# Optimization experiments

Measured on AMD Instinct MI355X. Metric: run time of the kernel, lower is better.

## Reference

```python
import jax, jax.numpy as jnp
import numpy as np

WAY = 5  # N_way from init


def setup_inputs() -> dict:
    key = jax.random.key(0)
    k1, k2, k3, k4 = jax.random.split(key, 4)
    N, c, h, w = 80, 2048, 16, 16
    S = 512  # shuffle_num
    x = jax.random.normal(k1, (N, c, h, w), dtype=jnp.float32)
    s_ca = jax.random.uniform(k2, (N, c, 1, 1), dtype=jnp.float32)
    # random channel indices per sample (stand-in for random.sample)
    rand_index = jax.random.randint(k3, (N, S), 0, c)
    # partner offset per sample (stand-in for random j != i)
    partner = jax.random.randint(k4, (N,), 0, N - 1)
    return {"x": x, "s_ca": s_ca, "rand_index": rand_index,
            "partner": partner, "shuffle_num": S}


def reference(x, s_ca, rand_index, partner, shuffle_num):
    N, c, h, w = x.shape
    way = WAY
    scores = s_ca.reshape(N, c)
    # per-sample top-k channels by attention score
    _, topk_idx = jax.lax.top_k(scores, shuffle_num)          # [N, S]
    # partner sample j != i (offset trick guarantees inequality)
    j = (jnp.arange(N) + 1 + partner) % N                      # [N]
    bi = jnp.arange(N)[:, None]                                # [N, 1]
    x_topk = x[bi, topk_idx]                                   # [N, S, h, w]
    x_part = x[j[:, None], rand_index]                         # [N, S, h, w]
    blend = 0.7 * x_topk + 0.3 * x_part
    # scatter blended channels back (batched gather-blend-scatter)
    aug_x = x.at[bi, topk_idx].set(blend)                      # [N, c, h, w]
    # group into (way, shot, ...) and concat original + augmented episodes
    x_r = x.reshape(way, -1, c, h, w)
    aug_r = aug_x.reshape(way, -1, c, h, w)
    out = jnp.concatenate((x_r, aug_r), axis=1)                # [way, 2*shot, c, h, w]
    s = s_ca.reshape(way, -1, c, 1, 1)
    s = jnp.concatenate((s, s), axis=1)                        # repeat(1,2,1,1,1)
    out = out * s
    return out.reshape(-1, c, h, w)                            # [2N, c, h, w]
```

## Files before the change

### kernel.cpp

```cpp
#include <hip/hip_runtime.h>

#define N_SAMP 80
#define C_CH   2048
#define HW     256
#define S_TOP  512
#define HW4    64

__global__ __launch_bounds__(256) void fused_shuffle_kernel(
    const float4* __restrict__ x4, const float* __restrict__ s_ca,
    const int* __restrict__ rand_index, const int* __restrict__ partner,
    float4* __restrict__ out4) {
  const unsigned int lane = threadIdx.x & 63u;
  const unsigned int wid = threadIdx.x >> 6;
  const unsigned int blk = blockIdx.x;
  const unsigned int n = blk >> 7;
  const unsigned int ch0 = ((blk & 127u) << 4) | (wid << 2);
  const unsigned int g = n >> 4;
  const unsigned int b = n & 15u;

  const float* __restrict__ row = s_ca + (size_t)n * C_CH;
  const float4* __restrict__ row4 = (const float4*)row;

  const float4 sq = row4[ch0 >> 2];
  const float si[4] = {sq.x, sq.y, sq.z, sq.w};

  int jn = (int)n + 1 + partner[n];
  if (jn >= N_SAMP) jn -= N_SAMP;

  float4 v[4];
#pragma unroll
  for (int c = 0; c < 4; ++c)
    v[c] = x4[(((size_t)n * C_CH + ch0 + c) << 6) | lane];

  unsigned long long kc[4];
#pragma unroll
  for (int c = 0; c < 4; ++c) {
    unsigned int bi = __float_as_uint(si[c]);
    bi ^= (bi & 0x80000000u) ? 0xFFFFFFFFu : 0x80000000u;
    kc[c] = ((unsigned long long)bi << 11) |
            (unsigned long long)(C_CH - 1 - (ch0 + c));
  }

  int cnt[4] = {0, 0, 0, 0};
#pragma unroll
  for (int q = 0; q < 8; ++q) {
    const float4 sv = row4[q * 64 + lane];
    const unsigned int j0 = 4u * (q * 64u + lane);
    unsigned long long kj[4];
#pragma unroll
    for (int e = 0; e < 4; ++e) {
      unsigned int bj = __float_as_uint((&sv.x)[e]);
      bj ^= (bj & 0x80000000u) ? 0xFFFFFFFFu : 0x80000000u;
      kj[e] = ((unsigned long long)bj << 11) |
              (unsigned long long)(C_CH - 1 - (j0 + e));
    }
#pragma unroll
    for (int c = 0; c < 4; ++c) {
#pragma unroll
      for (int e = 0; e < 4; ++e)
        cnt[c] += __popcll(__ballot(kj[e] > kc[c]));
    }
  }

  const size_t base_plain =
      (((size_t)((g << 5) | b) * C_CH + ch0) << 6) | lane;
  const size_t aug_off = ((size_t)(16 * C_CH)) << 6;

#pragma unroll
  for (int c = 0; c < 4; ++c) {
    const float s = si[c];
    float4 pv = make_float4(v[c].x * s, v[c].y * s, v[c].z * s, v[c].w * s);
    float4 av = pv;
    if (cnt[c] < S_TOP) {
      const int pc = rand_index[(size_t)n * S_TOP + cnt[c]];
      const float4 u = x4[((((size_t)jn << 11) | (size_t)pc) << 6) | lane];
      av.x = (0.7f * v[c].x + 0.3f * u.x) * s;
      av.y = (0.7f * v[c].y + 0.3f * u.y) * s;
      av.z = (0.7f * v[c].z + 0.3f * u.z) * s;
      av.w = (0.7f * v[c].w + 0.3f * u.w) * s;
    }
    out4[base_plain + ((size_t)c << 6)] = pv;
    out4[base_plain + aug_off + ((size_t)c << 6)] = av;
  }
}

extern "C" void kernel_launch(void* const* d_in, const int* in_sizes, int n_in,
                              void* d_out, int out_size, void* d_ws,
                              size_t ws_size, hipStream_t stream) {
  const float* x = (const float*)d_in[0];
  const float* s_ca = (const float*)d_in[1];
  const int* rand_index = (const int*)d_in[2];
  const int* partner = (const int*)d_in[3];

  const int nblocks = (N_SAMP * C_CH) / 16;
  fused_shuffle_kernel<<<nblocks, 256, 0, stream>>>(
      (const float4*)x, s_ca, rand_index, partner, (float4*)d_out);
}
```

Before: 445.7 us.

## Precompute per-sample top-k ranks via histogram bucket sort in a separate kernel

Moves the per-channel rank computation out of the streaming kernel into a per-sample kernel that buckets scores by value, sorts within buckets in shared memory, and writes a channel-to-partner-channel map to workspace. The streaming kernel then reads one index per channel instead of doing 128 wave ballots per wave. This removes redundant O(C) rank work repeated by every wave, at the cost of an extra launch and a low-parallelism 80-block prologue. Bucketing assumes scores spread over [0,1) for balanced buckets, but it remains correct for any values.

```diff
diff --git a/kernel.cpp b/kernel.cpp
--- a/kernel.cpp
+++ b/kernel.cpp
@@ -6,9 +6,91 @@
 #define S_TOP  512
 #define HW4    64
 
-__global__ __launch_bounds__(256) void fused_shuffle_kernel(
+__global__ __launch_bounds__(256) void rank_hist_kernel(
+    const float* __restrict__ s_ca, const int* __restrict__ rand_index,
+    int* __restrict__ pcmap) {
+  __shared__ unsigned int keys[C_CH];
+  __shared__ unsigned short bkt[C_CH];
+  __shared__ int hist[C_CH];
+  __shared__ int cumgt[C_CH];
+  __shared__ unsigned long long sorted[C_CH];
+  __shared__ int chunk[256];
+
+  const int n = blockIdx.x;
+  const int t = threadIdx.x;
+  const float* __restrict__ row = s_ca + (size_t)n * C_CH;
+
+  for (int i = t; i < C_CH; i += 256) hist[i] = 0;
+  __syncthreads();
+
+  for (int i = t; i < C_CH; i += 256) {
+    const float s = row[i];
+    unsigned int mb = __float_as_uint(s);
+    mb ^= (mb & 0x80000000u) ? 0xFFFFFFFFu : 0x80000000u;
+    keys[i] = mb;
+    int b = (int)(s * 2048.0f);
+    b = (b < 0) ? 0 : ((b > 2047) ? 2047 : b);
+    bkt[i] = (unsigned short)b;
+    atomicAdd(&hist[b], 1);
+  }
+  __syncthreads();
+
+  {
+    int cs = 0;
+#pragma unroll
+    for (int k = 0; k < 8; ++k) cs += hist[t * 8 + k];
+    chunk[t] = cs;
+  }
+  __syncthreads();
+  for (int d = 1; d < 256; d <<= 1) {
+    const int add = (t >= d) ? chunk[t - d] : 0;
+    __syncthreads();
+    chunk[t] += add;
+    __syncthreads();
+  }
+  const int total = chunk[255];
+
+  {
+    int run = total - chunk[t];
+#pragma unroll
+    for (int k = 7; k >= 0; --k) {
+      cumgt[t * 8 + k] = run;
+      run += hist[t * 8 + k];
+    }
+  }
+  __syncthreads();
+
+  for (int i = t; i < C_CH; i += 256) hist[i] = 0;
+  __syncthreads();
+
+  for (int i = t; i < C_CH; i += 256) {
+    const int b = bkt[i];
+    const unsigned long long key =
+        ((unsigned long long)keys[i] << 11) |
+        (unsigned long long)(C_CH - 1 - i);
+    const int pos = cumgt[b] + atomicAdd(&hist[b], 1);
+    sorted[pos] = key;
+  }
+  __syncthreads();
+
+  int* __restrict__ pm = pcmap + (size_t)n * C_CH;
+  const int* __restrict__ ri = rand_index + (size_t)n * S_TOP;
+  for (int i = t; i < C_CH; i += 256) {
+    const int b = bkt[i];
+    const int lo = cumgt[b];
+    const int nb = ((b > 0) ? cumgt[b - 1] : total) - lo;
+    const unsigned long long mykey =
+        ((unsigned long long)keys[i] << 11) |
+        (unsigned long long)(C_CH - 1 - i);
+    int r = lo;
+    for (int p = lo; p < lo + nb; ++p) r += (sorted[p] > mykey) ? 1 : 0;
+    pm[i] = (r < S_TOP) ? ri[r] : -1;
+  }
+}
+
+__global__ __launch_bounds__(256) void stream_out_kernel(
     const float4* __restrict__ x4, const float* __restrict__ s_ca,
-    const int* __restrict__ rand_index, const int* __restrict__ partner,
+    const int* __restrict__ pcmap, const int* __restrict__ partner,
     float4* __restrict__ out4) {
   const unsigned int lane = threadIdx.x & 63u;
   const unsigned int wid = threadIdx.x >> 6;
@@ -18,49 +100,20 @@
   const unsigned int g = n >> 4;
   const unsigned int b = n & 15u;
 
-  const float* __restrict__ row = s_ca + (size_t)n * C_CH;
-  const float4* __restrict__ row4 = (const float4*)row;
-
-  const float4 sq = row4[ch0 >> 2];
+  const float4 sq = ((const float4*)(s_ca + (size_t)n * C_CH))[ch0 >> 2];
   const float si[4] = {sq.x, sq.y, sq.z, sq.w};
 
   int jn = (int)n + 1 + partner[n];
   if (jn >= N_SAMP) jn -= N_SAMP;
 
+  int pc[4];
+#pragma unroll
+  for (int c = 0; c < 4; ++c) pc[c] = pcmap[(size_t)n * C_CH + ch0 + c];
+
   float4 v[4];
 #pragma unroll
   for (int c = 0; c < 4; ++c)
     v[c] = x4[(((size_t)n * C_CH + ch0 + c) << 6) | lane];
-
-  unsigned long long kc[4];
-#pragma unroll
-  for (int c = 0; c < 4; ++c) {
-    unsigned int bi = __float_as_uint(si[c]);
-    bi ^= (bi & 0x80000000u) ? 0xFFFFFFFFu : 0x80000000u;
-    kc[c] = ((unsigned long long)bi << 11) |
-            (unsigned long long)(C_CH - 1 - (ch0 + c));
-  }
-
-  int cnt[4] = {0, 0, 0, 0};
-#pragma unroll
-  for (int q = 0; q < 8; ++q) {
-    const float4 sv = row4[q * 64 + lane];
-    const unsigned int j0 = 4u * (q * 64u + lane);
-    unsigned long long kj[4];
-#pragma unroll
-    for (int e = 0; e < 4; ++e) {
-      unsigned int bj = __float_as_uint((&sv.x)[e]);
-      bj ^= (bj & 0x80000000u) ? 0xFFFFFFFFu : 0x80000000u;
-      kj[e] = ((unsigned long long)bj << 11) |
-              (unsigned long long)(C_CH - 1 - (j0 + e));
-    }
-#pragma unroll
-    for (int c = 0; c < 4; ++c) {
-#pragma unroll
-      for (int e = 0; e < 4; ++e)
-        cnt[c] += __popcll(__ballot(kj[e] > kc[c]));
-    }
-  }
 
   const size_t base_plain =
       (((size_t)((g << 5) | b) * C_CH + ch0) << 6) | lane;
@@ -71,9 +124,9 @@
     const float s = si[c];
     float4 pv = make_float4(v[c].x * s, v[c].y * s, v[c].z * s, v[c].w * s);
     float4 av = pv;
-    if (cnt[c] < S_TOP) {
-      const int pc = rand_index[(size_t)n * S_TOP + cnt[c]];
-      const float4 u = x4[((((size_t)jn << 11) | (size_t)pc) << 6) | lane];
+    if (pc[c] >= 0) {
+      const float4 u =
+          x4[((((size_t)jn << 11) | (size_t)pc[c]) << 6) | lane];
       av.x = (0.7f * v[c].x + 0.3f * u.x) * s;
       av.y = (0.7f * v[c].y + 0.3f * u.y) * s;
       av.z = (0.7f * v[c].z + 0.3f * u.z) * s;
@@ -92,7 +145,11 @@
   const int* rand_index = (const int*)d_in[2];
   const int* partner = (const int*)d_in[3];
 
+  int* pcmap = (int*)d_ws;
+
+  rank_hist_kernel<<<N_SAMP, 256, 0, stream>>>(s_ca, rand_index, pcmap);
+
   const int nblocks = (N_SAMP * C_CH) / 16;
-  fused_shuffle_kernel<<<nblocks, 256, 0, stream>>>(
-      (const float4*)x, s_ca, rand_index, partner, (float4*)d_out);
+  stream_out_kernel<<<nblocks, 256, 0, stream>>>(
+      (const float4*)x, s_ca, pcmap, partner, (float4*)d_out);
 }
```

After: 447.6 us. About the same (+0.4%).
